# Kernel tuning notes

Measured on AMD Instinct MI355X. Metric: run time of the kernel, lower is better.

The kernel has to match this reference:

```python
import jax, jax.numpy as jnp
import numpy as np

B, N, L, C, H, W = 4, 5, 5, 64, 100, 252
DISCRETE_RATIO = 0.4  # voxel_size[0]
DOWNSAMPLE_RATE = 2


def setup_inputs() -> dict:
    key = jax.random.key(0)
    k1, k2, k3, k4 = jax.random.split(key, 4)
    x = jax.random.normal(k1, (B * N, C, H, W), dtype=jnp.float32)
    confidence_map = jax.random.uniform(k2, (B * N, 1, H, W), dtype=jnp.float32)
    record_len = jnp.full((B,), N, dtype=jnp.int32)
    # realistic SE(2)-in-SE(3) pairwise transforms: small rotation + translation
    theta = jax.random.uniform(k3, (B, L, L), minval=-0.1, maxval=0.1)
    txy = jax.random.uniform(k4, (B, L, L, 2), minval=-5.0, maxval=5.0)
    c, s = jnp.cos(theta), jnp.sin(theta)
    z, o = jnp.zeros_like(theta), jnp.ones_like(theta)
    T = jnp.stack([
        jnp.stack([c, -s, z, txy[..., 0]], -1),
        jnp.stack([s, c, z, txy[..., 1]], -1),
        jnp.stack([z, z, o, z], -1),
        jnp.stack([z, z, z, o], -1),
    ], -2).astype(jnp.float32)  # (B, L, L, 4, 4)
    return {"x": x, "confidence_map": confidence_map,
            "record_len": record_len, "pairwise_t_matrix": T}


def _normalize_affine(T, Hh, Ww):
    # rows [0,1], cols [0,1,3] -> (B,L,L,2,3), then normalize per module code
    M = T[:, :, :, jnp.array([0, 1])][:, :, :, :, jnp.array([0, 1, 3])]
    scale = jnp.array(
        [[1.0, Hh / Ww, 2.0 / (DOWNSAMPLE_RATE * DISCRETE_RATIO * Ww)],
         [Ww / Hh, 1.0, 2.0 / (DOWNSAMPLE_RATE * DISCRETE_RATIO * Hh)]],
        dtype=T.dtype)
    return M * scale


def _sample(img, grid):
    # img (C,H,W); grid (Ni,H,W,2) normalized coords, align_corners=True,
    # bilinear, zeros padding (matches torch affine_grid+grid_sample)
    Hh, Ww = img.shape[-2:]
    ix = (grid[..., 0] + 1.0) * 0.5 * (Ww - 1)
    iy = (grid[..., 1] + 1.0) * 0.5 * (Hh - 1)
    x0f, y0f = jnp.floor(ix), jnp.floor(iy)
    x0, y0 = x0f.astype(jnp.int32), y0f.astype(jnp.int32)
    x1, y1 = x0 + 1, y0 + 1
    wx1, wy1 = ix - x0f, iy - y0f
    wx0, wy0 = 1.0 - wx1, 1.0 - wy1

    def g(yy, xx):
        valid = ((xx >= 0) & (xx < Ww) & (yy >= 0) & (yy < Hh)).astype(img.dtype)
        v = img[:, jnp.clip(yy, 0, Hh - 1), jnp.clip(xx, 0, Ww - 1)]  # (C,Ni,H,W)
        return v * valid

    out = (g(y0, x0) * (wy0 * wx0) + g(y0, x1) * (wy0 * wx1)
           + g(y1, x0) * (wy1 * wx0) + g(y1, x1) * (wy1 * wx1))
    return jnp.moveaxis(out, 0, 1)  # (Ni,C,H,W)


def _forward(x, pairwise_t_matrix):
    BN, Cc, Hh, Ww = x.shape
    Bb = pairwise_t_matrix.shape[0]
    Nn = BN // Bb  # uniform record_len
    M = _normalize_affine(pairwise_t_matrix, Hh, Ww)[:, :Nn, :Nn]  # (B,N,N,2,3)
    feats = x.reshape(Bb, Nn, Cc, Hh, Ww)
    xs = jnp.linspace(-1.0, 1.0, Ww)
    ys = jnp.linspace(-1.0, 1.0, Hh)
    gx, gy = jnp.meshgrid(xs, ys)  # (H,W)
    base = jnp.stack([gx, gy, jnp.ones_like(gx)], -1)  # (H,W,3)

    def fuse_batch(feats_b, M_b):
        # M_b[i, j] warps neighbor j's feature into ego i's frame
        coords = jnp.einsum('ijkc,hwc->ijhwk', M_b, base)  # (Ni,Nj,H,W,2)
        warped = jax.vmap(_sample, in_axes=(0, 1))(feats_b, coords)  # (Nj,Ni,C,H,W)
        return warped.max(axis=0)  # max-fuse over neighbors -> (Ni,C,H,W)

    fused = jax.vmap(fuse_batch)(feats, M)  # (B,N,C,H,W)
    return fused.reshape(BN, Cc, Hh, Ww)


def reference(x, confidence_map, record_len, pairwise_t_matrix):
    # communication=False path: confidence_map unused, comm rate = 0
    return _forward(x, pairwise_t_matrix)
```

## Files before the change

### kernel.cpp

```cpp
#include <hip/hip_runtime.h>
#include <math.h>

#define BB 4
#define NN 5
#define CC 64
#define HH 100
#define WW 252
#define HW (HH * WW)
#define TILE_W 64
#define NTW ((WW + TILE_W - 1) / TILE_W)
#define NXCD 8
#define PAD_B (64 * 1024)
#define PAD_A (128 * 1024)

typedef _Float16 h2v __attribute__((ext_vector_type(2)));
typedef _Float16 h8v __attribute__((ext_vector_type(8)));

__global__ __launch_bounds__(256) void transpose_chw_hwc(
    const float* __restrict__ x, _Float16* __restrict__ xt)
{
    __shared__ float tile[CC][TILE_W + 1];
    const int blk = blockIdx.x;
    const int wt  = blk % NTW;
    const int h   = (blk / NTW) % HH;
    const int bn  = blk / (NTW * HH);
    const int w0  = wt * TILE_W;

    const int lane = threadIdx.x & 63;
    const int sub  = threadIdx.x >> 6;

#pragma unroll
    for (int it = 0; it < 16; ++it) {
        const int c = sub + 4 * it;
        const int w = w0 + lane;
        if (w < WW)
            tile[c][lane] = x[((size_t)(bn * CC + c) * HH + h) * WW + w];
    }
    __syncthreads();
#pragma unroll
    for (int it = 0; it < 8; ++it) {
        const int unit = it * 256 + threadIdx.x;
        const int px = unit >> 5;
        const int c2 = unit & 31;
        const int w  = w0 + px;
        if (w < WW) {
            h2v hv;
            hv[0] = (_Float16)tile[2 * c2 + 0][px];
            hv[1] = (_Float16)tile[2 * c2 + 1][px];
            *(h2v*)(xt + ((((size_t)bn * HH + h) * WW + w) * CC + 2 * c2)) = hv;
        }
    }
}

__global__ __launch_bounds__(512) void fuse_gather(
    const _Float16* __restrict__ xt,
    const float* __restrict__ T,
    float* __restrict__ out)
{
    __shared__ float coord[NN][TILE_W][5];
    __shared__ float tile[TILE_W][CC + 1];

    const int cpx = gridDim.x / NXCD;
    const int blk = (blockIdx.x % NXCD) * cpx + blockIdx.x / NXCD;

    const int wt  = blk % NTW;
    const int h   = (blk / NTW) % HH;
    const int bi  = blk / (NTW * HH);
    const int b   = bi / NN;
    const int i   = bi % NN;
    const int w0  = wt * TILE_W;

    const int lane = threadIdx.x & 63;
    const int wv   = threadIdx.x >> 6;

    if (wv < NN) {
        const int jj = wv;
        const int w  = w0 + lane;
        const float gx = -1.0f + 2.0f * (float)w / (float)(WW - 1);
        const float gy = -1.0f + 2.0f * (float)h / (float)(HH - 1);
        const float sHW = (float)HH / (float)WW;
        const float sWH = (float)WW / (float)HH;
        const float sW  = 2.5f / (float)WW;
        const float sH  = 2.5f / (float)HH;

        const float* Tm = T + ((size_t)(b * NN + i) * NN + jj) * 16;
        const float m00 = Tm[0];
        const float m01 = Tm[1] * sHW;
        const float m02 = Tm[3] * sW;
        const float m10 = Tm[4] * sWH;
        const float m11 = Tm[5];
        const float m12 = Tm[7] * sH;

        const float cx = __builtin_fmaf(m00, gx, __builtin_fmaf(m01, gy, m02));
        const float cy = __builtin_fmaf(m10, gx, __builtin_fmaf(m11, gy, m12));
        const float ix = (cx + 1.0f) * (0.5f * (float)(WW - 1));
        const float iy = (cy + 1.0f) * (0.5f * (float)(HH - 1));

        const float x0f = floorf(ix);
        const float y0f = floorf(iy);
        const int x0 = (int)x0f, y0 = (int)y0f;
        const int x1 = x0 + 1,  y1 = y0 + 1;

        const float wx1 = ix - x0f, wy1 = iy - y0f;
        const float wx0 = 1.0f - wx1, wy0 = 1.0f - wy1;

        const float v00 = (x0 >= 0 && x0 < WW && y0 >= 0 && y0 < HH) ? 1.0f : 0.0f;
        const float v01 = (x1 >= 0 && x1 < WW && y0 >= 0 && y0 < HH) ? 1.0f : 0.0f;
        const float v10 = (x0 >= 0 && x0 < WW && y1 >= 0 && y1 < HH) ? 1.0f : 0.0f;
        const float v11 = (x1 >= 0 && x1 < WW && y1 >= 0 && y1 < HH) ? 1.0f : 0.0f;

        const int x0s = min(max(x0, -1), WW);
        const int y0s = min(max(y0, -1), HH);
        const int oc  = (y0s * WW + x0s) * CC;

        float* cd = coord[jj][lane];
        cd[0] = __int_as_float(oc);
        cd[1] = wy0 * wx0 * v00;
        cd[2] = wy0 * wx1 * v01;
        cd[3] = wy1 * wx0 * v10;
        cd[4] = wy1 * wx1 * v11;
    }
    __syncthreads();

    {
        const int g   = lane >> 3;
        const int ch8 = (lane & 7) * 8;
        const int p   = wv * 8 + g;

        if (w0 + p < WW) {
            float a0 = -INFINITY, a1 = -INFINITY, a2 = -INFINITY, a3 = -INFINITY;
            float a4 = -INFINITY, a5 = -INFINITY, a6 = -INFINITY, a7 = -INFINITY;

#pragma unroll
            for (int j = 0; j < NN; ++j) {
                const float* cd = coord[j][p];
                const int   oc  = __float_as_int(cd[0]);
                const float w00 = cd[1], w01 = cd[2], w10 = cd[3], w11 = cd[4];

                const _Float16* base0 = xt + (size_t)(b * NN + j) * HW * CC
                                           + (long)oc + ch8;
                const _Float16* base1 = base0 + (long)WW * CC;

                const h8v t00 = *(const h8v*)(base0);
                const h8v t01 = *(const h8v*)(base0 + CC);
                const h8v t10 = *(const h8v*)(base1);
                const h8v t11 = *(const h8v*)(base1 + CC);

                float s;
                s = __builtin_fmaf(w00, (float)t00[0], __builtin_fmaf(w01, (float)t01[0],
                    __builtin_fmaf(w10, (float)t10[0], w11 * (float)t11[0])));
                a0 = fmaxf(a0, s);
                s = __builtin_fmaf(w00, (float)t00[1], __builtin_fmaf(w01, (float)t01[1],
                    __builtin_fmaf(w10, (float)t10[1], w11 * (float)t11[1])));
                a1 = fmaxf(a1, s);
                s = __builtin_fmaf(w00, (float)t00[2], __builtin_fmaf(w01, (float)t01[2],
                    __builtin_fmaf(w10, (float)t10[2], w11 * (float)t11[2])));
                a2 = fmaxf(a2, s);
                s = __builtin_fmaf(w00, (float)t00[3], __builtin_fmaf(w01, (float)t01[3],
                    __builtin_fmaf(w10, (float)t10[3], w11 * (float)t11[3])));
                a3 = fmaxf(a3, s);
                s = __builtin_fmaf(w00, (float)t00[4], __builtin_fmaf(w01, (float)t01[4],
                    __builtin_fmaf(w10, (float)t10[4], w11 * (float)t11[4])));
                a4 = fmaxf(a4, s);
                s = __builtin_fmaf(w00, (float)t00[5], __builtin_fmaf(w01, (float)t01[5],
                    __builtin_fmaf(w10, (float)t10[5], w11 * (float)t11[5])));
                a5 = fmaxf(a5, s);
                s = __builtin_fmaf(w00, (float)t00[6], __builtin_fmaf(w01, (float)t01[6],
                    __builtin_fmaf(w10, (float)t10[6], w11 * (float)t11[6])));
                a6 = fmaxf(a6, s);
                s = __builtin_fmaf(w00, (float)t00[7], __builtin_fmaf(w01, (float)t01[7],
                    __builtin_fmaf(w10, (float)t10[7], w11 * (float)t11[7])));
                a7 = fmaxf(a7, s);
            }
            float* tp = &tile[p][ch8];
            tp[0] = a0; tp[1] = a1; tp[2] = a2; tp[3] = a3;
            tp[4] = a4; tp[5] = a5; tp[6] = a6; tp[7] = a7;
        }
    }
    __syncthreads();

#pragma unroll
    for (int rep = 0; rep < 2; ++rep) {
        const int unit = threadIdx.x + 512 * rep;
        const int q = unit & 15;
        const int c = unit >> 4;
        const int w = w0 + 4 * q;
        if (w < WW) {
            float4 v;
            v.x = tile[4 * q + 0][c];
            v.y = tile[4 * q + 1][c];
            v.z = tile[4 * q + 2][c];
            v.w = tile[4 * q + 3][c];
            *(float4*)(out + ((size_t)bi * CC + c) * HW + h * WW + w) = v;
        }
    }
}

#define CG 16
#define NCG (CC / CG)
__global__ __launch_bounds__(256, 4) void where2comm_fuse_fallback(
    const float* __restrict__ x, const float* __restrict__ T,
    float* __restrict__ out)
{
    const int tid = blockIdx.x * blockDim.x + threadIdx.x;
    const int total = BB * NN * HW * NCG;
    if (tid >= total) return;
    const int w = tid % WW;
    int t2 = tid / WW;
    const int h = t2 % HH;
    t2 /= HH;
    const int bi = t2 % (BB * NN);
    const int cg = t2 / (BB * NN);
    const int b = bi / NN, i = bi % NN;
    const float gx = -1.0f + 2.0f * (float)w / (float)(WW - 1);
    const float gy = -1.0f + 2.0f * (float)h / (float)(HH - 1);
    float acc[CG];
#pragma unroll
    for (int c = 0; c < CG; ++c) acc[c] = -INFINITY;
    const float sHW = (float)HH / (float)WW, sWH = (float)WW / (float)HH;
    const float sW = 2.5f / (float)WW, sH = 2.5f / (float)HH;
    for (int j = 0; j < NN; ++j) {
        const float* Tm = T + ((size_t)(b * NN + i) * NN + j) * 16;
        const float m00 = Tm[0], m01 = Tm[1] * sHW, m02 = Tm[3] * sW;
        const float m10 = Tm[4] * sWH, m11 = Tm[5], m12 = Tm[7] * sH;
        const float cx = __builtin_fmaf(m00, gx, __builtin_fmaf(m01, gy, m02));
        const float cy = __builtin_fmaf(m10, gx, __builtin_fmaf(m11, gy, m12));
        const float ix = (cx + 1.0f) * (0.5f * (float)(WW - 1));
        const float iy = (cy + 1.0f) * (0.5f * (float)(HH - 1));
        const float x0f = floorf(ix), y0f = floorf(iy);
        const int x0 = (int)x0f, y0 = (int)y0f, x1 = x0 + 1, y1 = y0 + 1;
        const float wx1 = ix - x0f, wy1 = iy - y0f;
        const float wx0 = 1.0f - wx1, wy0 = 1.0f - wy1;
        const float v00 = (x0 >= 0 && x0 < WW && y0 >= 0 && y0 < HH) ? 1.0f : 0.0f;
        const float v01 = (x1 >= 0 && x1 < WW && y0 >= 0 && y0 < HH) ? 1.0f : 0.0f;
        const float v10 = (x0 >= 0 && x0 < WW && y1 >= 0 && y1 < HH) ? 1.0f : 0.0f;
        const float v11 = (x1 >= 0 && x1 < WW && y1 >= 0 && y1 < HH) ? 1.0f : 0.0f;
        const float w00 = wy0 * wx0 * v00, w01 = wy0 * wx1 * v01;
        const float w10 = wy1 * wx0 * v10, w11 = wy1 * wx1 * v11;
        const int x0c = min(max(x0, 0), WW - 1), x1c = min(max(x1, 0), WW - 1);
        const int y0c = min(max(y0, 0), HH - 1), y1c = min(max(y1, 0), HH - 1);
        const int o00 = y0c * WW + x0c, o01 = y0c * WW + x1c;
        const int o10 = y1c * WW + x0c, o11 = y1c * WW + x1c;
        const float* p = x + ((size_t)(b * NN + j) * CC + cg * CG) * HW;
        float t00[CG], t01[CG], t10[CG], t11[CG];
#pragma unroll
        for (int c = 0; c < CG; ++c) {
            const float* pc = p + (size_t)c * HW;
            t00[c] = pc[o00]; t01[c] = pc[o01]; t10[c] = pc[o10]; t11[c] = pc[o11];
        }
#pragma unroll
        for (int c = 0; c < CG; ++c) {
            const float s = __builtin_fmaf(w00, t00[c], __builtin_fmaf(w01, t01[c],
                            __builtin_fmaf(w10, t10[c], w11 * t11[c])));
            acc[c] = fmaxf(acc[c], s);
        }
    }
    float* op = out + ((size_t)bi * CC + cg * CG) * HW + h * WW + w;
#pragma unroll
    for (int c = 0; c < CG; ++c) op[(size_t)c * HW] = acc[c];
}

extern "C" void kernel_launch(void* const* d_in, const int* in_sizes, int n_in,
                              void* d_out, int out_size, void* d_ws, size_t ws_size,
                              hipStream_t stream) {
    const float* x = (const float*)d_in[0];
    const float* T = (const float*)d_in[3];
    float* out = (float*)d_out;

    const size_t xt_bytes = (size_t)BB * NN * HH * WW * CC * sizeof(_Float16);
    if (ws_size >= PAD_B + xt_bytes + PAD_A) {
        _Float16* xt = (_Float16*)((char*)d_ws + PAD_B);
        const int grid1 = BB * NN * HH * NTW;
        transpose_chw_hwc<<<grid1, 256, 0, stream>>>(x, xt);
        const int grid2 = BB * NN * HH * NTW;
        fuse_gather<<<grid2, 512, 0, stream>>>(xt, T, out);
    } else {
        const int total = BB * NN * HW * NCG;
        where2comm_fuse_fallback<<<(total + 255) / 256, 256, 0, stream>>>(x, T, out);
    }
}
```

Before: 109.3 us.

## Use packed fp16 bilinear math and reorder block index for neighbor locality

The bilinear interpolation and max-fuse now run in packed half-precision (h2v) FMAs instead of converting every fp16 sample to fp32, with the weights stored pre-packed as fp16 pairs in shared memory. This roughly halves the ALU instruction count and removes the conversions in the inner loop. Separately, the block index decomposition is changed so that the ego index i varies fastest, which is meant to make consecutive blocks on the same XCD read overlapping neighbor rows for L2 reuse. The cost is reduced accumulation precision: fp16 weights and sums can drift from the fp32 reference.

```diff
diff --git a/kernel.cpp b/kernel.cpp
--- a/kernel.cpp
+++ b/kernel.cpp
@@ -63,11 +63,13 @@
     const int cpx = gridDim.x / NXCD;
     const int blk = (blockIdx.x % NXCD) * cpx + blockIdx.x / NXCD;
 
-    const int wt  = blk % NTW;
-    const int h   = (blk / NTW) % HH;
-    const int bi  = blk / (NTW * HH);
-    const int b   = bi / NN;
-    const int i   = bi % NN;
+    const int b   = blk / (NN * HH * NTW);
+    const int r   = blk % (NN * HH * NTW);
+    const int i   = r % NN;
+    const int hwt = r / NN;
+    const int wt  = hwt % NTW;
+    const int h   = hwt / NTW;
+    const int bi  = b * NN + i;
     const int w0  = wt * TILE_W;
 
     const int lane = threadIdx.x & 63;
@@ -113,12 +115,17 @@
         const int y0s = min(max(y0, -1), HH);
         const int oc  = (y0s * WW + x0s) * CC;
 
+        const _Float16 h00 = (_Float16)(wy0 * wx0 * v00);
+        const _Float16 h01 = (_Float16)(wy0 * wx1 * v01);
+        const _Float16 h10 = (_Float16)(wy1 * wx0 * v10);
+        const _Float16 h11 = (_Float16)(wy1 * wx1 * v11);
+
         float* cd = coord[jj][lane];
         cd[0] = __int_as_float(oc);
-        cd[1] = wy0 * wx0 * v00;
-        cd[2] = wy0 * wx1 * v01;
-        cd[3] = wy1 * wx0 * v10;
-        cd[4] = wy1 * wx1 * v11;
+        h2v p00 = {h00, h00}; cd[1] = __builtin_bit_cast(float, p00);
+        h2v p01 = {h01, h01}; cd[2] = __builtin_bit_cast(float, p01);
+        h2v p10 = {h10, h10}; cd[3] = __builtin_bit_cast(float, p10);
+        h2v p11 = {h11, h11}; cd[4] = __builtin_bit_cast(float, p11);
     }
     __syncthreads();
 
@@ -128,14 +135,17 @@
         const int p   = wv * 8 + g;
 
         if (w0 + p < WW) {
-            float a0 = -INFINITY, a1 = -INFINITY, a2 = -INFINITY, a3 = -INFINITY;
-            float a4 = -INFINITY, a5 = -INFINITY, a6 = -INFINITY, a7 = -INFINITY;
+            const _Float16 NEGINF = (_Float16)(-INFINITY);
+            h2v a0 = {NEGINF, NEGINF}, a1 = a0, a2 = a0, a3 = a0;
 
 #pragma unroll
             for (int j = 0; j < NN; ++j) {
                 const float* cd = coord[j][p];
-                const int   oc  = __float_as_int(cd[0]);
-                const float w00 = cd[1], w01 = cd[2], w10 = cd[3], w11 = cd[4];
+                const int oc  = __float_as_int(cd[0]);
+                const h2v w00 = __builtin_bit_cast(h2v, cd[1]);
+                const h2v w01 = __builtin_bit_cast(h2v, cd[2]);
+                const h2v w10 = __builtin_bit_cast(h2v, cd[3]);
+                const h2v w11 = __builtin_bit_cast(h2v, cd[4]);
 
                 const _Float16* base0 = xt + (size_t)(b * NN + j) * HW * CC
                                            + (long)oc + ch8;
@@ -146,35 +156,26 @@
                 const h8v t10 = *(const h8v*)(base1);
                 const h8v t11 = *(const h8v*)(base1 + CC);
 
-                float s;
-                s = __builtin_fmaf(w00, (float)t00[0], __builtin_fmaf(w01, (float)t01[0],
-                    __builtin_fmaf(w10, (float)t10[0], w11 * (float)t11[0])));
-                a0 = fmaxf(a0, s);
-                s = __builtin_fmaf(w00, (float)t00[1], __builtin_fmaf(w01, (float)t01[1],
-                    __builtin_fmaf(w10, (float)t10[1], w11 * (float)t11[1])));
-                a1 = fmaxf(a1, s);
-                s = __builtin_fmaf(w00, (float)t00[2], __builtin_fmaf(w01, (float)t01[2],
-                    __builtin_fmaf(w10, (float)t10[2], w11 * (float)t11[2])));
-                a2 = fmaxf(a2, s);
-                s = __builtin_fmaf(w00, (float)t00[3], __builtin_fmaf(w01, (float)t01[3],
-                    __builtin_fmaf(w10, (float)t10[3], w11 * (float)t11[3])));
-                a3 = fmaxf(a3, s);
-                s = __builtin_fmaf(w00, (float)t00[4], __builtin_fmaf(w01, (float)t01[4],
-                    __builtin_fmaf(w10, (float)t10[4], w11 * (float)t11[4])));
-                a4 = fmaxf(a4, s);
-                s = __builtin_fmaf(w00, (float)t00[5], __builtin_fmaf(w01, (float)t01[5],
-                    __builtin_fmaf(w10, (float)t10[5], w11 * (float)t11[5])));
-                a5 = fmaxf(a5, s);
-                s = __builtin_fmaf(w00, (float)t00[6], __builtin_fmaf(w01, (float)t01[6],
-                    __builtin_fmaf(w10, (float)t10[6], w11 * (float)t11[6])));
-                a6 = fmaxf(a6, s);
-                s = __builtin_fmaf(w00, (float)t00[7], __builtin_fmaf(w01, (float)t01[7],
-                    __builtin_fmaf(w10, (float)t10[7], w11 * (float)t11[7])));
-                a7 = fmaxf(a7, s);
+#define CHUNK(k, acc)                                                          \
+                {                                                              \
+                    h2v c00 = __builtin_shufflevector(t00, t00, 2*k, 2*k+1);   \
+                    h2v c01 = __builtin_shufflevector(t01, t01, 2*k, 2*k+1);   \
+                    h2v c10 = __builtin_shufflevector(t10, t10, 2*k, 2*k+1);   \
+                    h2v c11 = __builtin_shufflevector(t11, t11, 2*k, 2*k+1);   \
+                    h2v s = c11 * w11;                                         \
+                    s = c10 * w10 + s;                                         \
+                    s = c01 * w01 + s;                                         \
+                    s = c00 * w00 + s;                                         \
+                    acc = __builtin_elementwise_max(acc, s);                   \
+                }
+                CHUNK(0, a0) CHUNK(1, a1) CHUNK(2, a2) CHUNK(3, a3)
+#undef CHUNK
             }
             float* tp = &tile[p][ch8];
-            tp[0] = a0; tp[1] = a1; tp[2] = a2; tp[3] = a3;
-            tp[4] = a4; tp[5] = a5; tp[6] = a6; tp[7] = a7;
+            tp[0] = (float)a0[0]; tp[1] = (float)a0[1];
+            tp[2] = (float)a1[0]; tp[3] = (float)a1[1];
+            tp[4] = (float)a2[0]; tp[5] = (float)a2[1];
+            tp[6] = (float)a3[0]; tp[7] = (float)a3[1];
         }
     }
     __syncthreads();
```

Measured after the change: 101.2 us. 7.4% less time.
